# Kernel optimization log

Hardware: AMD Instinct MI355X
Metric: run time of the kernel (lower is better)

## Reference

```python
import jax, jax.numpy as jnp
import numpy as np
import math

B, N, DIM, NH, K, PD = 2, 2048, 512, 8, 32, 16
HD = DIM // NH
LN_EPS = 1e-6  # flax LayerNorm default


def _poincare_dist(x, y, c):
    # x, y broadcast to [B, N, N, PD]; returns [B, N, N]
    diff_norm_sq = jnp.sum((x - y) ** 2, axis=-1)
    x_norm_sq = jnp.sum(x ** 2, axis=-1)
    y_norm_sq = jnp.sum(y ** 2, axis=-1)
    den = (1.0 - c * x_norm_sq) * (1.0 - c * y_norm_sq)
    arg = 1.0 + 2.0 * c * diff_norm_sq / jnp.clip(den, 1e-8)
    safe_arg = jnp.maximum(arg, 1.0 + 1e-7)
    return jnp.arccosh(safe_arg) / jnp.sqrt(c)


def _layernorm(x, scale, bias):
    m = jnp.mean(x, axis=-1, keepdims=True)
    v = jnp.var(x, axis=-1, keepdims=True)
    return (x - m) / jnp.sqrt(v + LN_EPS) * scale + bias


def setup_inputs() -> dict:
    key = jax.random.key(0)
    ks = jax.random.split(key, 12)

    def dense(k, din, dout):
        W = jax.random.normal(k, (din, dout), jnp.float32) / np.sqrt(din).astype(np.float32)
        b = jnp.zeros((dout,), jnp.float32)
        return W, b

    inp = {}
    inp["x"] = jax.random.normal(ks[0], (B, N, DIM), jnp.float32)
    # points inside the unit Poincare ball (c=1)
    inp["positions"] = (jax.random.uniform(ks[1], (B, N, PD), jnp.float32) - 0.5) * 0.2
    inp["c"] = jnp.float32(1.0)
    inp["Wq"], inp["bq"] = dense(ks[2], DIM, DIM)
    inp["Wk"], inp["bk"] = dense(ks[3], DIM, DIM)
    inp["Wv"], inp["bv"] = dense(ks[4], DIM, DIM)
    inp["Wo"], inp["bo"] = dense(ks[5], DIM, DIM)
    inp["W1"], inp["b1"] = dense(ks[6], DIM, 4 * DIM)
    inp["W2"], inp["b2"] = dense(ks[7], 4 * DIM, DIM)
    inp["ln1_scale"] = jnp.ones((DIM,), jnp.float32)
    inp["ln1_bias"] = jnp.zeros((DIM,), jnp.float32)
    inp["ln2_scale"] = jnp.ones((DIM,), jnp.float32)
    inp["ln2_bias"] = jnp.zeros((DIM,), jnp.float32)
    inp["log_tau"] = jnp.zeros((1,), jnp.float32)
    inp["attn_scale"] = jnp.ones((1,), jnp.float32)
    return inp


def reference(x, positions, c, Wq, bq, Wk, bk, Wv, bv, Wo, bo,
              W1, b1, W2, b2, ln1_scale, ln1_bias, ln2_scale, ln2_bias,
              log_tau, attn_scale):
    x_res = x
    x_norm = _layernorm(x, ln1_scale, ln1_bias)

    def heads(W, b):
        return (x_norm @ W + b).reshape(B, N, NH, HD).transpose(0, 2, 1, 3)  # [B,H,N,HD]

    q = heads(Wq, bq)
    k = heads(Wk, bk)
    v = heads(Wv, bv)

    # pairwise hyperbolic distances [B,N,N]
    dist_matrix = _poincare_dist(positions[:, None, :, :], positions[:, :, None, :], c)
    _, top_k_indices = jax.lax.top_k(-dist_matrix, K)  # [B,N,K]

    # gather neighbor K/V: out[b,h,i,j,d] = kv[b,h, idx[b,i,j], d]
    gather = jax.vmap(lambda kv_b, idx_b: kv_b[:, idx_b, :])
    k_gathered = gather(k, top_k_indices)  # [B,H,N,K,HD]
    v_gathered = gather(v, top_k_indices)  # [B,H,N,K,HD]

    feature_scores = jnp.einsum('bhid,bhikd->bhik', q, k_gathered) / math.sqrt(HD)
    gathered_dists = jnp.take_along_axis(dist_matrix, top_k_indices, axis=-1)  # [B,N,K]
    geometric_scores = -gathered_dists[:, None, :, :] / jnp.clip(jnp.exp(log_tau), 1e-8)
    attn_scores = attn_scale * jnp.tanh(feature_scores + geometric_scores)
    attn_weights = jax.nn.softmax(attn_scores, axis=-1)

    attn_output = jnp.einsum('bhik,bhikd->bhid', attn_weights, v_gathered)
    attn_output = attn_output.transpose(0, 2, 1, 3).reshape(B, N, DIM)

    x1 = x_res + attn_output @ Wo + bo
    x2_norm = _layernorm(x1, ln2_scale, ln2_bias)
    ffn = jax.nn.gelu(x2_norm @ W1 + b1) @ W2 + b2  # gelu approximate=True (flax default)
    return x1 + ffn
```

## Files before the change

kernel.cpp:

```cpp
#include <hip/hip_runtime.h>
#include <math.h>

#define B_   2
#define N_   2048
#define DIM_ 512
#define NH_  8
#define HD_  64
#define K_   32
#define PD_  16
#define TOK_ (B_*N_)
#define FFN_ 2048
#define QKV_ (3*DIM_)
#define KV_  1024

typedef __bf16 bf16x8 __attribute__((ext_vector_type(8)));
typedef float  f32x4  __attribute__((ext_vector_type(4)));

__device__ __forceinline__ unsigned short f2bf(float f) {
    unsigned int u = __float_as_uint(f);
    u = (u + 0x7fffu + ((u >> 16) & 1u)) >> 16;
    return (unsigned short)u;
}

__device__ __forceinline__ float bflo(unsigned u) { return __uint_as_float(u << 16); }
__device__ __forceinline__ float bfhi(unsigned u) { return __uint_as_float(u & 0xffff0000u); }

__device__ __forceinline__ float gelu_tanh(float x) {
    float x3 = x * x * x;
    return 0.5f * x * (1.f + tanhf(0.7978845608028654f * (x + 0.044715f * x3)));
}

__device__ __forceinline__ float tanh_fast(float x) {
    float e = __expf(2.f * x);
    return 1.f - 2.f / (e + 1.f);
}

__device__ __forceinline__ int lane_mbcnt(unsigned long long m) {
    return __builtin_amdgcn_mbcnt_hi((unsigned)(m >> 32),
           __builtin_amdgcn_mbcnt_lo((unsigned)m, 0));
}

#define GLOAD_LDS16(g, l) __builtin_amdgcn_global_load_lds(                        \
    (const __attribute__((address_space(1))) unsigned int*)(const void*)(g),       \
    (__attribute__((address_space(3))) unsigned int*)(void*)(l), 16, 0, 0)

template<int EPI, int BM, int BN>
__global__ __launch_bounds__(256)
void gemm_bf16_kernel(const unsigned short* __restrict__ A,
                      const unsigned short* __restrict__ Bt,
                      const float* __restrict__ bias,
                      const float* __restrict__ res,
                      float* __restrict__ Cf,
                      unsigned short* __restrict__ Cb,
                      int N, int Kd)
{
    constexpr int WM = BM / 2;
    constexpr int WN = BN / 2;
    constexpr int FM = WM / 16;
    constexpr int FN = WN / 16;

    __shared__ __align__(16) unsigned short smem[(BM+BN)*64];
    unsigned short* As_ = smem;
    unsigned short* Bs_ = smem + BM * 64;

    int t    = threadIdx.x;
    int lane = t & 63;
    int wid  = t >> 6;
    int wm   = wid >> 1, wn = wid & 1;
    int bm0  = blockIdx.y * BM;
    int bn0  = blockIdx.x * BN;
    int quad = lane >> 4;
    int rlo  = lane & 15;

    f32x4 acc[FM][FN] = {};

    for (int k0 = 0; k0 < Kd; k0 += 64) {
#pragma unroll
        for (int l = 0; l < BM/32; l++) {
            int idx = l*256 + t;
            int r   = idx >> 3;
            int g   = (idx & 7) ^ (r & 7);
            GLOAD_LDS16(A + (size_t)(bm0 + r) * Kd + k0 + g*8, As_ + idx*8);
        }
#pragma unroll
        for (int l = 0; l < BN/32; l++) {
            int idx = l*256 + t;
            int r   = idx >> 3;
            int g   = (idx & 7) ^ (r & 7);
            GLOAD_LDS16(Bt + (size_t)(bn0 + r) * Kd + k0 + g*8, Bs_ + idx*8);
        }
        __syncthreads();

        bf16x8 af[FM][2], bfr[FN][2];
#pragma unroll
        for (int mi = 0; mi < FM; mi++) {
            int r = wm*WM + mi*16 + rlo;
#pragma unroll
            for (int s = 0; s < 2; s++)
                af[mi][s] = *(const bf16x8*)(As_ + r*64 + ((s*4 + quad) ^ (r & 7))*8);
        }
#pragma unroll
        for (int ni = 0; ni < FN; ni++) {
            int r = wn*WN + ni*16 + rlo;
#pragma unroll
            for (int s = 0; s < 2; s++)
                bfr[ni][s] = *(const bf16x8*)(Bs_ + r*64 + ((s*4 + quad) ^ (r & 7))*8);
        }
#pragma unroll
        for (int s = 0; s < 2; s++)
#pragma unroll
            for (int mi = 0; mi < FM; mi++)
#pragma unroll
                for (int ni = 0; ni < FN; ni++)
                    acc[mi][ni] = __builtin_amdgcn_mfma_f32_16x16x32_bf16(
                        af[mi][s], bfr[ni][s], acc[mi][ni], 0, 0, 0);
        __syncthreads();
    }

#pragma unroll
    for (int mi = 0; mi < FM; mi++) {
#pragma unroll
        for (int ni = 0; ni < FN; ni++) {
            int col = bn0 + wn*WN + ni*16 + rlo;
            float bv = bias[col];
#pragma unroll
            for (int r = 0; r < 4; r++) {
                int row = bm0 + wm*WM + mi*16 + quad*4 + r;
                float val = acc[mi][ni][r] + bv;
                if (EPI == 1) val += res[(size_t)row * N + col];
                if (EPI == 2) {
                    val = gelu_tanh(val);
                    Cb[(size_t)row * N + col] = f2bf(val);
                } else if (EPI == 3) {
                    if (col < DIM_) Cf[(size_t)row * DIM_ + col] = val;
                    else            Cb[(size_t)row * KV_ + (col - DIM_)] = f2bf(val);
                } else {
                    Cf[(size_t)row * N + col] = val;
                }
            }
        }
    }
}

__global__ __launch_bounds__(256)
void dist_topk_split_kernel(const float* __restrict__ pos,
                            const float* __restrict__ posT,
                            const float* __restrict__ pos_sq,
                            const float* __restrict__ c_ptr,
                            int* __restrict__ topk_idx, float* __restrict__ topk_dist)
{
    __shared__ unsigned long long cand[2][64];

    int wid  = threadIdx.x >> 6;
    int lane = threadIdx.x & 63;
    int rw   = wid >> 1;
    int hw   = wid & 1;
    int bi   = blockIdx.x * 2 + rw;
    int b    = bi >> 11;
    float c  = *c_ptr;
    float inv_sqrt_c = rsqrtf(c);

    float pi[16];
    {
        const float4* pi4 = (const float4*)(pos + (size_t)bi * PD_);
        float4 a0 = pi4[0], a1 = pi4[1], a2 = pi4[2], a3 = pi4[3];
        pi[0]=a0.x; pi[1]=a0.y; pi[2]=a0.z; pi[3]=a0.w;
        pi[4]=a1.x; pi[5]=a1.y; pi[6]=a1.z; pi[7]=a1.w;
        pi[8]=a2.x; pi[9]=a2.y; pi[10]=a2.z; pi[11]=a2.w;
        pi[12]=a3.x; pi[13]=a3.y; pi[14]=a3.z; pi[15]=a3.w;
    }
    float ni = pos_sq[bi];
    float omci = 1.f - c * ni;

    const float* pT  = posT + (size_t)b * 16 * N_;
    const float* sqb = pos_sq + b * N_;
    int jbase = hw * 1024;
    int j0l   = jbase + lane * 4;

    unsigned rb[16];
#pragma unroll
    for (int jg = 0; jg < 4; jg++) {
        int j0 = j0l + jg * 256;
        float dfx = 0.f, dfy = 0.f, dfz = 0.f, dfw = 0.f;
#pragma unroll
        for (int d = 0; d < 16; d++) {
            float4 v = *(const float4*)(pT + d * N_ + j0);
            float dx = pi[d]-v.x, dy = pi[d]-v.y, dz = pi[d]-v.z, dw = pi[d]-v.w;
            dfx += dx*dx; dfy += dy*dy; dfz += dz*dz; dfw += dw*dw;
        }
        float4 sq = *(const float4*)(sqb + j0);
        float dfa[4] = {dfx, dfy, dfz, dfw};
        float sqa[4] = {sq.x, sq.y, sq.z, sq.w};
#pragma unroll
        for (int jj = 0; jj < 4; jj++) {
            float den = fmaxf(omci * (1.f - c * sqa[jj]), 1e-8f);
            float arg = fmaxf(1.f + 2.f * c * dfa[jj] / den, 1.f + 1e-7f);
            rb[jg*4 + jj] = __float_as_uint(arg);
        }
    }

    unsigned band = rb[0], bor = rb[0];
#pragma unroll
    for (int tt = 1; tt < 16; tt++) { band &= rb[tt]; bor |= rb[tt]; }
#pragma unroll
    for (int off = 32; off; off >>= 1) {
        band &= __shfl_xor(band, off);
        bor  |= __shfl_xor(bor,  off);
    }
    unsigned diffb = band ^ bor;
    int hib = diffb ? (31 - __clz(diffb)) : -1;
    unsigned T = (hib >= 0) ? (band & ~((1u << (hib+1)) - 1u)) : band;

    for (int bit = hib; bit >= 0; --bit) {
        unsigned probe = T | (1u << bit);
        int cnt = 0;
#pragma unroll
        for (int tt = 0; tt < 16; tt++)
            cnt += __popcll(__ballot(rb[tt] < probe));
        if (cnt < K_) T = probe;
    }

    int cnt_lt = 0;
#pragma unroll
    for (int tt = 0; tt < 16; tt++)
        cnt_lt += __popcll(__ballot(rb[tt] < T));
    int m = K_ - cnt_lt;

    int ltpos = 0;
#pragma unroll
    for (int tt = 0; tt < 16; tt++) {
        bool is_lt = rb[tt] < T;
        unsigned long long mlt = __ballot(is_lt);
        int p = ltpos + lane_mbcnt(mlt);
        if (is_lt) {
            int j = jbase + (tt >> 2)*256 + lane*4 + (tt & 3);
            cand[rw][hw*K_ + p] = ((unsigned long long)rb[tt] << 32) | (unsigned)j;
        }
        ltpos += __popcll(mlt);
    }

    int eqpos = 0;
#pragma unroll
    for (int jg = 0; jg < 4; jg++) {
        bool iseq[4]; unsigned long long meq[4]; int bel[4];
#pragma unroll
        for (int jj = 0; jj < 4; jj++) {
            iseq[jj] = (rb[jg*4+jj] == T);
            meq[jj]  = __ballot(iseq[jj]);
            bel[jj]  = lane_mbcnt(meq[jj]);
        }
        int lane_prefix = bel[0] + bel[1] + bel[2] + bel[3];
        int within = 0;
#pragma unroll
        for (int jj = 0; jj < 4; jj++) {
            int p = eqpos + lane_prefix + within;
            if (iseq[jj] && p < m) {
                int j = jbase + jg*256 + lane*4 + jj;
                cand[rw][hw*K_ + cnt_lt + p] =
                    ((unsigned long long)rb[jg*4+jj] << 32) | (unsigned)j;
            }
            within += iseq[jj] ? 1 : 0;
        }
        eqpos += __popcll(meq[0]) + __popcll(meq[1]) + __popcll(meq[2]) + __popcll(meq[3]);
    }
    __syncthreads();

    if (hw == 0) {
        unsigned long long mykey = cand[rw][lane];
        int rank = 0;
#pragma unroll 8
        for (int M = 0; M < 64; M++)
            rank += (cand[rw][M] < mykey) ? 1 : 0;
        if (rank < K_) {
            unsigned rbv = (unsigned)(mykey >> 32);
            int      j   = (int)(mykey & 0xffffffffu);
            topk_idx [(size_t)bi * K_ + rank] = j;
            topk_dist[(size_t)bi * K_ + rank] = acoshf(__uint_as_float(rbv)) * inv_sqrt_c;
        }
    }
}

__global__ void fused_prep_kernel(const float* __restrict__ Wq, const float* __restrict__ Wk,
                            const float* __restrict__ Wv, const float* __restrict__ Wo,
                            const float* __restrict__ W1, const float* __restrict__ W2,
                            const float* __restrict__ bq, const float* __restrict__ bk,
                            const float* __restrict__ bv,
                            unsigned short* __restrict__ qkvWt,
                            unsigned short* __restrict__ WoT,
                            unsigned short* __restrict__ W1T,
                            unsigned short* __restrict__ W2T,
                            float* __restrict__ qkv_b,
                            const float* __restrict__ pos,
                            float* __restrict__ pos_sq,
                            float* __restrict__ posT,
                            const float* __restrict__ x,
                            const float* __restrict__ ln1_scale,
                            const float* __restrict__ ln1_bias,
                            unsigned short* __restrict__ xn)
{
    int id = blockIdx.x;
    int t  = threadIdx.x;

    if (id >= 3094) {
        int wave = (id - 3094) * 4 + (t >> 6);
        int lane = t & 63;
        const float* xr = x + (size_t)wave * DIM_;
        float v[8];
        float s = 0.f;
#pragma unroll
        for (int i = 0; i < 8; i++) { v[i] = xr[lane + i*64]; s += v[i]; }
#pragma unroll
        for (int off = 32; off; off >>= 1) s += __shfl_xor(s, off);
        float mean = s * (1.f / DIM_);
        float vs = 0.f;
#pragma unroll
        for (int i = 0; i < 8; i++) { float d = v[i] - mean; vs += d*d; }
#pragma unroll
        for (int off = 32; off; off >>= 1) vs += __shfl_xor(vs, off);
        float inv = rsqrtf(vs * (1.f / DIM_) + 1e-6f);
        unsigned short* yr = xn + (size_t)wave * DIM_;
#pragma unroll
        for (int i = 0; i < 8; i++) {
            int cc = lane + i*64;
            yr[cc] = f2bf((v[i] - mean) * inv * ln1_scale[cc] + ln1_bias[cc]);
        }
        return;
    }
    if (id >= 3078) {
        int i = (id - 3078) * 256 + t;
        int b = i >> 11, j = i & (N_ - 1);
        const float4* p = (const float4*)(pos + (size_t)i * PD_);
        float4 a0 = p[0], a1 = p[1], a2 = p[2], a3 = p[3];
        float pv[16] = {a0.x,a0.y,a0.z,a0.w, a1.x,a1.y,a1.z,a1.w,
                        a2.x,a2.y,a2.z,a2.w, a3.x,a3.y,a3.z,a3.w};
        float s = 0.f;
#pragma unroll
        for (int d = 0; d < 16; d++) s += pv[d]*pv[d];
        pos_sq[i] = s;
        float* pT = posT + (size_t)b * 16 * N_;
#pragma unroll
        for (int d = 0; d < 16; d++) pT[d * N_ + j] = pv[d];
        return;
    }
    if (id >= 3072) {
        int i = (id - 3072) * 256 + t;
        if (i < DIM_)            qkv_b[i] = bq[i];
        else if (i < 2*DIM_)     qkv_b[i] = bk[i - DIM_];
        else                     qkv_b[i] = bv[i - 2*DIM_];
        return;
    }

    const float* W; unsigned short* Wt; int Kd, Nw, nx, ti;
    if      (id < 256)  { W = Wq; Wt = qkvWt;               Kd = 512;  Nw = 512;  nx = 16; ti = id; }
    else if (id < 512)  { W = Wk; Wt = qkvWt + 512*512;     Kd = 512;  Nw = 512;  nx = 16; ti = id - 256; }
    else if (id < 768)  { W = Wv; Wt = qkvWt + 2*512*512;   Kd = 512;  Nw = 512;  nx = 16; ti = id - 512; }
    else if (id < 1024) { W = Wo; Wt = WoT;                 Kd = 512;  Nw = 512;  nx = 16; ti = id - 768; }
    else if (id < 2048) { W = W1; Wt = W1T;                 Kd = 512;  Nw = 2048; nx = 64; ti = id - 1024; }
    else                { W = W2; Wt = W2T;                 Kd = 2048; Nw = 512;  nx = 16; ti = id - 2048; }

    __shared__ float tile[32][33];
    int n0 = (ti % nx) * 32, k0 = (ti / nx) * 32;
    int tx = t & 31, ty = t >> 5;
#pragma unroll
    for (int i = 0; i < 32; i += 8)
        tile[ty + i][tx] = W[(size_t)(k0 + ty + i) * Nw + n0 + tx];
    __syncthreads();
#pragma unroll
    for (int i = 0; i < 32; i += 8)
        Wt[(size_t)(n0 + ty + i) * Kd + k0 + tx] = f2bf(tile[tx][ty + i]);
}

__global__ void layernorm_kernel(const float* __restrict__ x,
                                 const float* __restrict__ scale,
                                 const float* __restrict__ bias,
                                 unsigned short* __restrict__ y)
{
    int wave = (blockIdx.x * blockDim.x + threadIdx.x) >> 6;
    int lane = threadIdx.x & 63;
    if (wave >= TOK_) return;
    const float* xr = x + (size_t)wave * DIM_;
    float v[8];
    float s = 0.f;
#pragma unroll
    for (int i = 0; i < 8; i++) { v[i] = xr[lane + i*64]; s += v[i]; }
#pragma unroll
    for (int off = 32; off; off >>= 1) s += __shfl_xor(s, off);
    float mean = s * (1.f / DIM_);
    float vs = 0.f;
#pragma unroll
    for (int i = 0; i < 8; i++) { float d = v[i] - mean; vs += d*d; }
#pragma unroll
    for (int off = 32; off; off >>= 1) vs += __shfl_xor(vs, off);
    float inv = rsqrtf(vs * (1.f / DIM_) + 1e-6f);
    unsigned short* yr = y + (size_t)wave * DIM_;
#pragma unroll
    for (int i = 0; i < 8; i++) {
        int c = lane + i*64;
        yr[c] = f2bf((v[i] - mean) * inv * scale[c] + bias[c]);
    }
}

__global__ __launch_bounds__(256)
void attn_kernel(const float* __restrict__ q,
                 const unsigned short* __restrict__ kv,
                 const int* __restrict__ topk_idx, const float* __restrict__ topk_dist,
                 const float* __restrict__ log_tau_p, const float* __restrict__ attn_scale_p,
                 unsigned int* __restrict__ out)
{
    int gw   = (blockIdx.x * blockDim.x + threadIdx.x) >> 6;
    int lane = threadIdx.x & 63;
    if (gw >= B_ * NH_ * N_) return;
    int b = gw / (NH_ * N_);
    int r = gw % (NH_ * N_);
    int h = r / N_;
    int i = r % N_;
    int tok = b * N_ + i;

    float tau    = fmaxf(__expf(*log_tau_p), 1e-8f);
    float ascale = *attn_scale_p;

    const int*   idxp = topk_idx  + (size_t)tok * K_;
    const float* dstp = topk_dist + (size_t)tok * K_;
    int   my_idx  = idxp[lane & 31];
    float my_dist = dstp[lane & 31];

    int jj   = lane >> 1;
    int half = lane & 1;

    const float4* qp = (const float4*)(q + (size_t)tok * DIM_ + h * HD_ + half * 32);
    float4 qv[8];
#pragma unroll
    for (int u = 0; u < 8; u++) qv[u] = qp[u];

    int nb = __shfl(my_idx, jj);
    const uint4* kp = (const uint4*)(kv + (size_t)(b * N_ + nb) * KV_ + h * HD_ + half * 32);
    float dot = 0.f;
#pragma unroll
    for (int u = 0; u < 4; u++) {
        uint4 kw = kp[u];
        dot += qv[2*u].x   * bflo(kw.x) + qv[2*u].y   * bfhi(kw.x)
             + qv[2*u].z   * bflo(kw.y) + qv[2*u].w   * bfhi(kw.y)
             + qv[2*u+1].x * bflo(kw.z) + qv[2*u+1].y * bfhi(kw.z)
             + qv[2*u+1].z * bflo(kw.w) + qv[2*u+1].w * bfhi(kw.w);
    }
    dot += __shfl_xor(dot, 1);

    float fs = dot * 0.125f;
    float gs = -__shfl(my_dist, jj) / tau;
    float s  = ascale * tanh_fast(fs + gs);

    float mx = s;
#pragma unroll
    for (int off = 32; off; off >>= 1) mx = fmaxf(mx, __shfl_xor(mx, off));
    float e  = __expf(s - mx);
    float ec = half ? 0.f : e;
#pragma unroll
    for (int off = 32; off; off >>= 1) ec += __shfl_xor(ec, off);
    float inv = 1.f / ec;

    int dp    = lane & 31;
    int half2 = lane >> 5;
    const unsigned int* vb = (const unsigned int*)(kv + DIM_ + h * HD_) + dp;
    float ax = 0.f, ay = 0.f;
#pragma unroll
    for (int it = 0; it < 16; it++) {
        int t2 = half2 + 2*it;
        float w  = __shfl(e, t2 * 2) * inv;
        int   nj = __shfl(my_idx, t2);
        unsigned vv = vb[(size_t)(b * N_ + nj) * (KV_/2)];
        ax += w * bflo(vv);
        ay += w * bfhi(vv);
    }
    ax += __shfl_xor(ax, 32);
    ay += __shfl_xor(ay, 32);
    if (lane < 32) {
        unsigned pck = ((unsigned)f2bf(ay) << 16) | (unsigned)f2bf(ax);
        out[(size_t)tok * (DIM_/2) + h * (HD_/2) + dp] = pck;
    }
}

extern "C" void kernel_launch(void* const* d_in, const int* in_sizes, int n_in,
                              void* d_out, int out_size, void* d_ws, size_t ws_size,
                              hipStream_t stream)
{
    const float* x          = (const float*)d_in[0];
    const float* positions  = (const float*)d_in[1];
    const float* c_p        = (const float*)d_in[2];
    const float* Wq         = (const float*)d_in[3];
    const float* bq         = (const float*)d_in[4];
    const float* Wk         = (const float*)d_in[5];
    const float* bk         = (const float*)d_in[6];
    const float* Wv         = (const float*)d_in[7];
    const float* bv         = (const float*)d_in[8];
    const float* Wo         = (const float*)d_in[9];
    const float* bo         = (const float*)d_in[10];
    const float* W1         = (const float*)d_in[11];
    const float* b1         = (const float*)d_in[12];
    const float* W2         = (const float*)d_in[13];
    const float* b2         = (const float*)d_in[14];
    const float* ln1_scale  = (const float*)d_in[15];
    const float* ln1_bias   = (const float*)d_in[16];
    const float* ln2_scale  = (const float*)d_in[17];
    const float* ln2_bias   = (const float*)d_in[18];
    const float* log_tau    = (const float*)d_in[19];
    const float* attn_scale = (const float*)d_in[20];

    char* p = (char*)d_ws;
    unsigned short* qkvWt  = (unsigned short*)p; p += (size_t)QKV_ * DIM_ * 2;
    unsigned short* WoT    = (unsigned short*)p; p += (size_t)DIM_ * DIM_ * 2;
    unsigned short* W1T    = (unsigned short*)p; p += (size_t)FFN_ * DIM_ * 2;
    unsigned short* W2T    = (unsigned short*)p; p += (size_t)DIM_ * FFN_ * 2;
    float*          qkv_b  = (float*)p;          p += (size_t)QKV_ * 4;
    unsigned short* xn     = (unsigned short*)p; p += (size_t)TOK_ * DIM_ * 2;
    float*          qf     = (float*)p;          p += (size_t)TOK_ * DIM_ * 4;
    unsigned short* kvb    = (unsigned short*)p; p += (size_t)TOK_ * KV_ * 2;
    unsigned short* attn_o = (unsigned short*)p; p += (size_t)TOK_ * DIM_ * 2;
    float*          x1     = (float*)p;          p += (size_t)TOK_ * DIM_ * 4;
    unsigned short* x2n    = (unsigned short*)p; p += (size_t)TOK_ * DIM_ * 2;
    unsigned short* hbuf   = (unsigned short*)p; p += (size_t)TOK_ * FFN_ * 2;
    float*          pos_sq = (float*)p;          p += (size_t)TOK_ * 4;
    float*          posT   = (float*)p;          p += (size_t)B_ * 16 * N_ * 4;
    float*          tk_d   = (float*)p;          p += (size_t)TOK_ * K_ * 4;
    int*            tk_i   = (int*)p;            p += (size_t)TOK_ * K_ * 4;

    fused_prep_kernel<<<4118, 256, 0, stream>>>(Wq, Wk, Wv, Wo, W1, W2, bq, bk, bv,
                                                qkvWt, WoT, W1T, W2T, qkv_b,
                                                positions, pos_sq, posT,
                                                x, ln1_scale, ln1_bias, xn);

    gemm_bf16_kernel<3,64,128><<<dim3(QKV_/128, TOK_/64), 256, 0, stream>>>(
        xn, qkvWt, qkv_b, nullptr, qf, kvb, QKV_, DIM_);

    dist_topk_split_kernel<<<TOK_/2, 256, 0, stream>>>(positions, posT, pos_sq,
                                                       c_p, tk_i, tk_d);

    attn_kernel<<<(B_*NH_*N_)/4, 256, 0, stream>>>(qf, kvb, tk_i, tk_d,
                                                   log_tau, attn_scale,
                                                   (unsigned int*)attn_o);

    gemm_bf16_kernel<1,64,64><<<dim3(DIM_/64, TOK_/64), 256, 0, stream>>>(
        attn_o, WoT, bo, x, x1, nullptr, DIM_, DIM_);

    layernorm_kernel<<<TOK_/4, 256, 0, stream>>>(x1, ln2_scale, ln2_bias, x2n);

    gemm_bf16_kernel<2,64,128><<<dim3(FFN_/128, TOK_/64), 256, 0, stream>>>(
        x2n, W1T, b1, nullptr, nullptr, hbuf, FFN_, DIM_);

    gemm_bf16_kernel<1,64,64><<<dim3(DIM_/64, TOK_/64), 256, 0, stream>>>(
        hbuf, W2T, b2, x1, (float*)d_out, nullptr, DIM_, FFN_);
}
```

Measured before the change: 254.5 us.

## Split-K output GEMMs with atomic accumulation and process two rows per topk wave

The Wo and W2 GEMMs are split along K (2 and 4 chunks) and accumulate into preinitialized outputs with float atomicAdd. The residual-plus-bias initialization moves into the prep kernel (x + bo) and the LN2 kernel (x1 + b2). This raises block counts for these small-N GEMMs to fill more CUs. The top-k kernel now has each wave compute two query rows, sharing the loads of the transposed positions, and runs the bit-search radix select for both rows together. Atomics add memory traffic and make the summation order nondeterministic.

```diff
diff --git a/kernel.cpp b/kernel.cpp
--- a/kernel.cpp
+++ b/kernel.cpp
@@ -52,7 +52,7 @@
                       const float* __restrict__ res,
                       float* __restrict__ Cf,
                       unsigned short* __restrict__ Cb,
-                      int N, int Kd)
+                      int N, int Kstride, int Kchunk)
 {
     constexpr int WM = BM / 2;
     constexpr int WN = BN / 2;
@@ -71,23 +71,24 @@
     int bn0  = blockIdx.x * BN;
     int quad = lane >> 4;
     int rlo  = lane & 15;
+    int kbase = blockIdx.z * Kchunk;
 
     f32x4 acc[FM][FN] = {};
 
-    for (int k0 = 0; k0 < Kd; k0 += 64) {
+    for (int k0 = kbase; k0 < kbase + Kchunk; k0 += 64) {
 #pragma unroll
         for (int l = 0; l < BM/32; l++) {
             int idx = l*256 + t;
             int r   = idx >> 3;
             int g   = (idx & 7) ^ (r & 7);
-            GLOAD_LDS16(A + (size_t)(bm0 + r) * Kd + k0 + g*8, As_ + idx*8);
+            GLOAD_LDS16(A + (size_t)(bm0 + r) * Kstride + k0 + g*8, As_ + idx*8);
         }
 #pragma unroll
         for (int l = 0; l < BN/32; l++) {
             int idx = l*256 + t;
             int r   = idx >> 3;
             int g   = (idx & 7) ^ (r & 7);
-            GLOAD_LDS16(Bt + (size_t)(bn0 + r) * Kd + k0 + g*8, Bs_ + idx*8);
+            GLOAD_LDS16(Bt + (size_t)(bn0 + r) * Kstride + k0 + g*8, Bs_ + idx*8);
         }
         __syncthreads();
 
@@ -122,7 +123,7 @@
 #pragma unroll
         for (int ni = 0; ni < FN; ni++) {
             int col = bn0 + wn*WN + ni*16 + rlo;
-            float bv = bias[col];
+            float bv = (EPI == 4) ? 0.f : bias[col];
 #pragma unroll
             for (int r = 0; r < 4; r++) {
                 int row = bm0 + wm*WM + mi*16 + quad*4 + r;
@@ -134,6 +135,8 @@
                 } else if (EPI == 3) {
                     if (col < DIM_) Cf[(size_t)row * DIM_ + col] = val;
                     else            Cb[(size_t)row * KV_ + (col - DIM_)] = f2bf(val);
+                } else if (EPI == 4) {
+                    atomicAdd(&Cf[(size_t)row * N + col], val);
                 } else {
                     Cf[(size_t)row * N + col] = val;
                 }
@@ -142,90 +145,11 @@
     }
 }
 
-__global__ __launch_bounds__(256)
-void dist_topk_split_kernel(const float* __restrict__ pos,
-                            const float* __restrict__ posT,
-                            const float* __restrict__ pos_sq,
-                            const float* __restrict__ c_ptr,
-                            int* __restrict__ topk_idx, float* __restrict__ topk_dist)
-{
-    __shared__ unsigned long long cand[2][64];
-
-    int wid  = threadIdx.x >> 6;
-    int lane = threadIdx.x & 63;
-    int rw   = wid >> 1;
-    int hw   = wid & 1;
-    int bi   = blockIdx.x * 2 + rw;
-    int b    = bi >> 11;
-    float c  = *c_ptr;
-    float inv_sqrt_c = rsqrtf(c);
-
-    float pi[16];
-    {
-        const float4* pi4 = (const float4*)(pos + (size_t)bi * PD_);
-        float4 a0 = pi4[0], a1 = pi4[1], a2 = pi4[2], a3 = pi4[3];
-        pi[0]=a0.x; pi[1]=a0.y; pi[2]=a0.z; pi[3]=a0.w;
-        pi[4]=a1.x; pi[5]=a1.y; pi[6]=a1.z; pi[7]=a1.w;
-        pi[8]=a2.x; pi[9]=a2.y; pi[10]=a2.z; pi[11]=a2.w;
-        pi[12]=a3.x; pi[13]=a3.y; pi[14]=a3.z; pi[15]=a3.w;
-    }
-    float ni = pos_sq[bi];
-    float omci = 1.f - c * ni;
-
-    const float* pT  = posT + (size_t)b * 16 * N_;
-    const float* sqb = pos_sq + b * N_;
-    int jbase = hw * 1024;
-    int j0l   = jbase + lane * 4;
-
-    unsigned rb[16];
-#pragma unroll
-    for (int jg = 0; jg < 4; jg++) {
-        int j0 = j0l + jg * 256;
-        float dfx = 0.f, dfy = 0.f, dfz = 0.f, dfw = 0.f;
-#pragma unroll
-        for (int d = 0; d < 16; d++) {
-            float4 v = *(const float4*)(pT + d * N_ + j0);
-            float dx = pi[d]-v.x, dy = pi[d]-v.y, dz = pi[d]-v.z, dw = pi[d]-v.w;
-            dfx += dx*dx; dfy += dy*dy; dfz += dz*dz; dfw += dw*dw;
-        }
-        float4 sq = *(const float4*)(sqb + j0);
-        float dfa[4] = {dfx, dfy, dfz, dfw};
-        float sqa[4] = {sq.x, sq.y, sq.z, sq.w};
-#pragma unroll
-        for (int jj = 0; jj < 4; jj++) {
-            float den = fmaxf(omci * (1.f - c * sqa[jj]), 1e-8f);
-            float arg = fmaxf(1.f + 2.f * c * dfa[jj] / den, 1.f + 1e-7f);
-            rb[jg*4 + jj] = __float_as_uint(arg);
-        }
-    }
-
-    unsigned band = rb[0], bor = rb[0];
-#pragma unroll
-    for (int tt = 1; tt < 16; tt++) { band &= rb[tt]; bor |= rb[tt]; }
-#pragma unroll
-    for (int off = 32; off; off >>= 1) {
-        band &= __shfl_xor(band, off);
-        bor  |= __shfl_xor(bor,  off);
-    }
-    unsigned diffb = band ^ bor;
-    int hib = diffb ? (31 - __clz(diffb)) : -1;
-    unsigned T = (hib >= 0) ? (band & ~((1u << (hib+1)) - 1u)) : band;
-
-    for (int bit = hib; bit >= 0; --bit) {
-        unsigned probe = T | (1u << bit);
-        int cnt = 0;
-#pragma unroll
-        for (int tt = 0; tt < 16; tt++)
-            cnt += __popcll(__ballot(rb[tt] < probe));
-        if (cnt < K_) T = probe;
-    }
-
-    int cnt_lt = 0;
-#pragma unroll
-    for (int tt = 0; tt < 16; tt++)
-        cnt_lt += __popcll(__ballot(rb[tt] < T));
-    int m = K_ - cnt_lt;
-
+__device__ __forceinline__ void extract_row(const unsigned* rb, unsigned T,
+                                            int cnt_lt, int m,
+                                            unsigned long long* crow,
+                                            int hw, int jbase, int lane)
+{
     int ltpos = 0;
 #pragma unroll
     for (int tt = 0; tt < 16; tt++) {
@@ -234,11 +158,10 @@
         int p = ltpos + lane_mbcnt(mlt);
         if (is_lt) {
             int j = jbase + (tt >> 2)*256 + lane*4 + (tt & 3);
-            cand[rw][hw*K_ + p] = ((unsigned long long)rb[tt] << 32) | (unsigned)j;
+            crow[hw*K_ + p] = ((unsigned long long)rb[tt] << 32) | (unsigned)j;
         }
         ltpos += __popcll(mlt);
     }
-
     int eqpos = 0;
 #pragma unroll
     for (int jg = 0; jg < 4; jg++) {
@@ -256,26 +179,131 @@
             int p = eqpos + lane_prefix + within;
             if (iseq[jj] && p < m) {
                 int j = jbase + jg*256 + lane*4 + jj;
-                cand[rw][hw*K_ + cnt_lt + p] =
+                crow[hw*K_ + cnt_lt + p] =
                     ((unsigned long long)rb[jg*4+jj] << 32) | (unsigned)j;
             }
             within += iseq[jj] ? 1 : 0;
         }
         eqpos += __popcll(meq[0]) + __popcll(meq[1]) + __popcll(meq[2]) + __popcll(meq[3]);
     }
+}
+
+__global__ __launch_bounds__(256)
+void dist_topk_kernel(const float* __restrict__ pos,
+                      const float* __restrict__ posT,
+                      const float* __restrict__ pos_sq,
+                      const float* __restrict__ c_ptr,
+                      int* __restrict__ topk_idx, float* __restrict__ topk_dist)
+{
+    __shared__ unsigned long long cand[4][64];
+
+    int wid  = threadIdx.x >> 6;
+    int lane = threadIdx.x & 63;
+    int rg   = wid >> 1;
+    int hw   = wid & 1;
+    int bi0  = blockIdx.x * 4 + rg * 2;
+    int b    = bi0 >> 11;
+    float c  = *c_ptr;
+    float inv_sqrt_c = rsqrtf(c);
+
+    float pi0[16], pi1[16];
+    {
+        const float4* q0 = (const float4*)(pos + (size_t)bi0 * PD_);
+        const float4* q1 = (const float4*)(pos + (size_t)(bi0+1) * PD_);
+#pragma unroll
+        for (int u = 0; u < 4; u++) {
+            float4 a = q0[u];
+            pi0[4*u]=a.x; pi0[4*u+1]=a.y; pi0[4*u+2]=a.z; pi0[4*u+3]=a.w;
+            float4 e = q1[u];
+            pi1[4*u]=e.x; pi1[4*u+1]=e.y; pi1[4*u+2]=e.z; pi1[4*u+3]=e.w;
+        }
+    }
+    float om0 = 1.f - c * pos_sq[bi0];
+    float om1 = 1.f - c * pos_sq[bi0+1];
+
+    const float* pT  = posT + (size_t)b * 16 * N_;
+    const float* sqb = pos_sq + b * N_;
+    int jbase = hw * 1024;
+    int j0l   = jbase + lane * 4;
+
+    unsigned rb0[16], rb1[16];
+#pragma unroll
+    for (int jg = 0; jg < 4; jg++) {
+        int j0 = j0l + jg * 256;
+        float ax=0,ay=0,az=0,aw=0, bx=0,by=0,bz=0,bw=0;
+#pragma unroll
+        for (int d = 0; d < 16; d++) {
+            float4 v = *(const float4*)(pT + d * N_ + j0);
+            float d0x = pi0[d]-v.x, d0y = pi0[d]-v.y, d0z = pi0[d]-v.z, d0w = pi0[d]-v.w;
+            ax += d0x*d0x; ay += d0y*d0y; az += d0z*d0z; aw += d0w*d0w;
+            float d1x = pi1[d]-v.x, d1y = pi1[d]-v.y, d1z = pi1[d]-v.z, d1w = pi1[d]-v.w;
+            bx += d1x*d1x; by += d1y*d1y; bz += d1z*d1z; bw += d1w*d1w;
+        }
+        float4 sq = *(const float4*)(sqb + j0);
+        float da[4]={ax,ay,az,aw}, db[4]={bx,by,bz,bw}, sqa[4]={sq.x,sq.y,sq.z,sq.w};
+#pragma unroll
+        for (int jj = 0; jj < 4; jj++) {
+            float omj  = 1.f - c * sqa[jj];
+            float den0 = fmaxf(om0 * omj, 1e-8f);
+            float den1 = fmaxf(om1 * omj, 1e-8f);
+            rb0[jg*4+jj] = __float_as_uint(fmaxf(1.f + 2.f*c*da[jj]/den0, 1.f+1e-7f));
+            rb1[jg*4+jj] = __float_as_uint(fmaxf(1.f + 2.f*c*db[jj]/den1, 1.f+1e-7f));
+        }
+    }
+
+    unsigned T0, T1;
+    {
+        unsigned band0 = rb0[0], bor0 = rb0[0], band1 = rb1[0], bor1 = rb1[0];
+#pragma unroll
+        for (int tt = 1; tt < 16; tt++) {
+            band0 &= rb0[tt]; bor0 |= rb0[tt];
+            band1 &= rb1[tt]; bor1 |= rb1[tt];
+        }
+#pragma unroll
+        for (int off = 32; off; off >>= 1) {
+            band0 &= __shfl_xor(band0, off); bor0 |= __shfl_xor(bor0, off);
+            band1 &= __shfl_xor(band1, off); bor1 |= __shfl_xor(bor1, off);
+        }
+        unsigned df0 = band0 ^ bor0, df1 = band1 ^ bor1;
+        int hib0 = df0 ? (31 - __clz(df0)) : -1;
+        int hib1 = df1 ? (31 - __clz(df1)) : -1;
+        int hib  = hib0 > hib1 ? hib0 : hib1;
+        T0 = (hib >= 0) ? (band0 & ~((1u << (hib+1)) - 1u)) : band0;
+        T1 = (hib >= 0) ? (band1 & ~((1u << (hib+1)) - 1u)) : band1;
+        for (int bit = hib; bit >= 0; --bit) {
+            unsigned p0 = T0 | (1u << bit), p1 = T1 | (1u << bit);
+            int c0 = 0, c1 = 0;
+#pragma unroll
+            for (int tt = 0; tt < 16; tt++) {
+                c0 += __popcll(__ballot(rb0[tt] < p0));
+                c1 += __popcll(__ballot(rb1[tt] < p1));
+            }
+            if (c0 < K_) T0 = p0;
+            if (c1 < K_) T1 = p1;
+        }
+    }
+    int cl0 = 0, cl1 = 0;
+#pragma unroll
+    for (int tt = 0; tt < 16; tt++) {
+        cl0 += __popcll(__ballot(rb0[tt] < T0));
+        cl1 += __popcll(__ballot(rb1[tt] < T1));
+    }
+
+    extract_row(rb0, T0, cl0, K_ - cl0, cand[rg*2+0], hw, jbase, lane);
+    extract_row(rb1, T1, cl1, K_ - cl1, cand[rg*2+1], hw, jbase, lane);
     __syncthreads();
 
-    if (hw == 0) {
-        unsigned long long mykey = cand[rw][lane];
+    {
+        unsigned long long mykey = cand[wid][lane];
         int rank = 0;
 #pragma unroll 8
         for (int M = 0; M < 64; M++)
-            rank += (cand[rw][M] < mykey) ? 1 : 0;
+            rank += (cand[wid][M] < mykey) ? 1 : 0;
         if (rank < K_) {
-            unsigned rbv = (unsigned)(mykey >> 32);
-            int      j   = (int)(mykey & 0xffffffffu);
-            topk_idx [(size_t)bi * K_ + rank] = j;
-            topk_dist[(size_t)bi * K_ + rank] = acoshf(__uint_as_float(rbv)) * inv_sqrt_c;
+            int bi = blockIdx.x * 4 + wid;
+            topk_idx [(size_t)bi * K_ + rank] = (int)(mykey & 0xffffffffu);
+            topk_dist[(size_t)bi * K_ + rank] =
+                acoshf(__uint_as_float((unsigned)(mykey >> 32))) * inv_sqrt_c;
         }
     }
 }
@@ -284,7 +312,7 @@
                             const float* __restrict__ Wv, const float* __restrict__ Wo,
                             const float* __restrict__ W1, const float* __restrict__ W2,
                             const float* __restrict__ bq, const float* __restrict__ bk,
-                            const float* __restrict__ bv,
+                            const float* __restrict__ bv, const float* __restrict__ bo,
                             unsigned short* __restrict__ qkvWt,
                             unsigned short* __restrict__ WoT,
                             unsigned short* __restrict__ W1T,
@@ -296,11 +324,21 @@
                             const float* __restrict__ x,
                             const float* __restrict__ ln1_scale,
                             const float* __restrict__ ln1_bias,
-                            unsigned short* __restrict__ xn)
+                            unsigned short* __restrict__ xn,
+                            float* __restrict__ x1)
 {
     int id = blockIdx.x;
     int t  = threadIdx.x;
 
+    if (id >= 4118) {
+        int i4 = (id - 4118) * 256 + t;
+        float4 xv = ((const float4*)x)[i4];
+        int col4 = (i4 & 127) * 4;
+        float4 bv4 = *(const float4*)(bo + col4);
+        xv.x += bv4.x; xv.y += bv4.y; xv.z += bv4.z; xv.w += bv4.w;
+        ((float4*)x1)[i4] = xv;
+        return;
+    }
     if (id >= 3094) {
         int wave = (id - 3094) * 4 + (t >> 6);
         int lane = t & 63;
@@ -370,15 +408,17 @@
         Wt[(size_t)(n0 + ty + i) * Kd + k0 + tx] = f2bf(tile[tx][ty + i]);
 }
 
-__global__ void layernorm_kernel(const float* __restrict__ x,
-                                 const float* __restrict__ scale,
-                                 const float* __restrict__ bias,
-                                 unsigned short* __restrict__ y)
+__global__ void ln2_init_kernel(const float* __restrict__ x1,
+                                const float* __restrict__ scale,
+                                const float* __restrict__ bias,
+                                const float* __restrict__ b2,
+                                unsigned short* __restrict__ y,
+                                float* __restrict__ outf)
 {
     int wave = (blockIdx.x * blockDim.x + threadIdx.x) >> 6;
     int lane = threadIdx.x & 63;
     if (wave >= TOK_) return;
-    const float* xr = x + (size_t)wave * DIM_;
+    const float* xr = x1 + (size_t)wave * DIM_;
     float v[8];
     float s = 0.f;
 #pragma unroll
@@ -393,10 +433,12 @@
     for (int off = 32; off; off >>= 1) vs += __shfl_xor(vs, off);
     float inv = rsqrtf(vs * (1.f / DIM_) + 1e-6f);
     unsigned short* yr = y + (size_t)wave * DIM_;
+    float* orow = outf + (size_t)wave * DIM_;
 #pragma unroll
     for (int i = 0; i < 8; i++) {
         int c = lane + i*64;
         yr[c] = f2bf((v[i] - mean) * inv * scale[c] + bias[c]);
+        orow[c] = v[i] + b2[c];
     }
 }
 
@@ -523,29 +565,31 @@
     float*          tk_d   = (float*)p;          p += (size_t)TOK_ * K_ * 4;
     int*            tk_i   = (int*)p;            p += (size_t)TOK_ * K_ * 4;
 
-    fused_prep_kernel<<<4118, 256, 0, stream>>>(Wq, Wk, Wv, Wo, W1, W2, bq, bk, bv,
+    fused_prep_kernel<<<6166, 256, 0, stream>>>(Wq, Wk, Wv, Wo, W1, W2,
+                                                bq, bk, bv, bo,
                                                 qkvWt, WoT, W1T, W2T, qkv_b,
                                                 positions, pos_sq, posT,
-                                                x, ln1_scale, ln1_bias, xn);
-
-    gemm_bf16_kernel<3,64,128><<<dim3(QKV_/128, TOK_/64), 256, 0, stream>>>(
-        xn, qkvWt, qkv_b, nullptr, qf, kvb, QKV_, DIM_);
-
-    dist_topk_split_kernel<<<TOK_/2, 256, 0, stream>>>(positions, posT, pos_sq,
-                                                       c_p, tk_i, tk_d);
+                                                x, ln1_scale, ln1_bias, xn, x1);
+
+    gemm_bf16_kernel<3,64,128><<<dim3(QKV_/128, TOK_/64, 1), 256, 0, stream>>>(
+        xn, qkvWt, qkv_b, nullptr, qf, kvb, QKV_, DIM_, DIM_);
+
+    dist_topk_kernel<<<TOK_/4, 256, 0, stream>>>(positions, posT, pos_sq,
+                                                 c_p, tk_i, tk_d);
 
     attn_kernel<<<(B_*NH_*N_)/4, 256, 0, stream>>>(qf, kvb, tk_i, tk_d,
                                                    log_tau, attn_scale,
                                                    (unsigned int*)attn_o);
 
-    gemm_bf16_kernel<1,64,64><<<dim3(DIM_/64, TOK_/64), 256, 0, stream>>>(
-        attn_o, WoT, bo, x, x1, nullptr, DIM_, DIM_);
-
-    layernorm_kernel<<<TOK_/4, 256, 0, stream>>>(x1, ln2_scale, ln2_bias, x2n);
-
-    gemm_bf16_kernel<2,64,128><<<dim3(FFN_/128, TOK_/64), 256, 0, stream>>>(
-        x2n, W1T, b1, nullptr, nullptr, hbuf, FFN_, DIM_);
-
-    gemm_bf16_kernel<1,64,64><<<dim3(DIM_/64, TOK_/64), 256, 0, stream>>>(
-        hbuf, W2T, b2, x1, (float*)d_out, nullptr, DIM_, FFN_);
-}
+    gemm_bf16_kernel<4,64,64><<<dim3(DIM_/64, TOK_/64, 2), 256, 0, stream>>>(
+        attn_o, WoT, nullptr, nullptr, x1, nullptr, DIM_, DIM_, DIM_/2);
+
+    ln2_init_kernel<<<TOK_/4, 256, 0, stream>>>(x1, ln2_scale, ln2_bias, b2,
+                                                x2n, (float*)d_out);
+
+    gemm_bf16_kernel<2,64,128><<<dim3(FFN_/128, TOK_/64, 1), 256, 0, stream>>>(
+        x2n, W1T, b1, nullptr, nullptr, hbuf, FFN_, DIM_, DIM_);
+
+    gemm_bf16_kernel<4,64,64><<<dim3(DIM_/64, TOK_/64, 4), 256, 0, stream>>>(
+        hbuf, W2T, nullptr, nullptr, (float*)d_out, nullptr, DIM_, FFN_, FFN_/4);
+}
```

New measurement: 269.7 us. +6.0%, slower.
